# Kernel tuning notes

Hardware: AMD Instinct MI355X
Metric: run time of the kernel (lower is better)

Reference implementation:

```python
import jax, jax.numpy as jnp
import numpy as np

B, T, C, H = 2, 2048, 1024, 16
D = C // H  # head_dim = 64


def setup_inputs() -> dict:
    key = jax.random.key(0)
    k1, k2, k3, k4 = jax.random.split(key, 4)
    x = jax.random.normal(k1, (B, T, C), dtype=jnp.float32)
    # key_padding_mask: True for valid token, False for padding.
    # Use per-example valid lengths so the mask is realistic; every example
    # has length >= 1 so no softmax row is fully masked.
    lengths = jax.random.randint(k2, (B,), T // 2, T + 1)
    key_padding_mask = jnp.arange(T)[None, :] < lengths[:, None]
    Wqkv = jax.random.normal(k3, (3 * C, C), dtype=jnp.float32) * 0.02
    bqkv = jnp.zeros((3 * C,), dtype=jnp.float32)
    Wproj = jax.random.normal(k4, (C, C), dtype=jnp.float32) * 0.02
    bproj = jnp.zeros((C,), dtype=jnp.float32)
    return {"x": x, "key_padding_mask": key_padding_mask,
            "Wqkv": Wqkv, "bqkv": bqkv, "Wproj": Wproj, "bproj": bproj}


def reference(x, key_padding_mask, Wqkv, bqkv, Wproj, bproj):
    # qkv projection (torch Linear: y = x @ W^T + b)
    qkv = jnp.einsum('btc,oc->bto', x, Wqkv) + bqkv          # (B,T,3C)
    q, k, v = jnp.split(qkv, 3, axis=-1)
    q = q.reshape(B, T, H, D)
    k = k.reshape(B, T, H, D)
    v = v.reshape(B, T, H, D)
    scale = 1.0 / np.sqrt(D).astype(np.float32)
    scores = jnp.einsum('bqhd,bkhd->bhqk', q, k) * scale      # (B,H,T,T)
    causal = jnp.tril(jnp.ones((T, T), dtype=bool))           # (T,T)
    mask = causal[None, None, :, :] & key_padding_mask[:, None, None, :]
    scores = jnp.where(mask, scores, -jnp.inf)
    attn = jax.nn.softmax(scores, axis=-1)                    # dropout p=0.0
    out = jnp.einsum('bhqk,bkhd->bqhd', attn, v).reshape(B, T, C)
    out = jnp.einsum('btc,oc->bto', out, Wproj) + bproj
    return out
```

## Files before the change

### kernel.cpp

```cpp
#include <hip/hip_runtime.h>
#include <hip/hip_bf16.h>
#include <stdint.h>

#define B_ 2
#define T_ 2048
#define C_ 1024
#define H_ 16
#define D_ 64

typedef __attribute__((ext_vector_type(8))) short bf16x8;
typedef __attribute__((ext_vector_type(4))) float f32x4;

__device__ __forceinline__ unsigned short f2bf(float f) {
  union { float f; uint32_t u; } c; c.f = f;
  uint32_t r = c.u + 0x7FFFu + ((c.u >> 16) & 1u);
  return (unsigned short)(r >> 16);
}

__device__ __forceinline__ uint32_t pack_bf16x2(float lo, float hi) {
  uint32_t r;
  asm("v_cvt_pk_bf16_f32 %0, %1, %2" : "=v"(r) : "v"(lo), "v"(hi));
  return r;
}

__device__ __forceinline__ void gload_lds16(const unsigned short* g,
                                            unsigned short* l) {
  __builtin_amdgcn_global_load_lds(
      (const __attribute__((address_space(1))) void*)(g),
      (__attribute__((address_space(3))) void*)(l), 16, 0, 0);
}

__global__ void cvt_f32_bf16(const float* __restrict__ s,
                             unsigned short* __restrict__ d, int n4) {
  int i = blockIdx.x * blockDim.x + threadIdx.x;
  if (i >= n4) return;
  float4 v = ((const float4*)s)[i];
  ushort4 o;
  o.x = f2bf(v.x); o.y = f2bf(v.y); o.z = f2bf(v.z); o.w = f2bf(v.w);
  ((ushort4*)d)[i] = o;
}

__global__ void compute_lengths(const unsigned int* __restrict__ mask,
                                int* __restrict__ lens) {
  int lane = threadIdx.x;
  unsigned int w0 = mask[0];
  for (int b = 0; b < B_; ++b) {
    int cnt = 0;
    if (w0 == 1u) {
      for (int t = lane; t < T_; t += 64) cnt += (mask[(size_t)b * T_ + t] != 0u);
    } else if (w0 == 0x3F800000u) {
      const float* mf = (const float*)mask;
      for (int t = lane; t < T_; t += 64) cnt += (mf[(size_t)b * T_ + t] != 0.f);
    } else {
      const unsigned char* mb = (const unsigned char*)mask;
      for (int t = lane; t < T_; t += 64) cnt += (mb[(size_t)b * T_ + t] != 0);
    }
    for (int off = 32; off > 0; off >>= 1) cnt += __shfl_down(cnt, off);
    if (lane == 0) lens[b] = cnt;
  }
}

__global__ __launch_bounds__(256)
void gemm_bt(const unsigned short* __restrict__ A,
             const unsigned short* __restrict__ Bm,
             const float* __restrict__ bias,
             float* __restrict__ outF,
             unsigned short* __restrict__ Qw,
             unsigned short* __restrict__ Kw,
             unsigned short* __restrict__ Vw,
             int N, int K, int mode) {
  __shared__ unsigned short As[128 * 64];
  __shared__ unsigned short Bs[128 * 64];
  const int tid = threadIdx.x;
  const int lane = tid & 63;
  const int w = tid >> 6;
  const int wm = w >> 1, wn = w & 1;
  const int q4 = lane >> 4, l15 = lane & 15;
  const int bm = blockIdx.y * 128;
  const int bn = blockIdx.x * 128;

  f32x4 acc[4][4] = {};

  for (int kt = 0; kt < K; kt += 64) {
#pragma unroll
    for (int i = 0; i < 4; ++i) {
      int r0 = w * 32 + i * 8;
      int row = r0 + (lane >> 3);
      int kc = (lane & 7) ^ (row & 7);
      gload_lds16(A + (size_t)(bm + row) * K + kt + kc * 8, &As[r0 * 64]);
      gload_lds16(Bm + (size_t)(bn + row) * K + kt + kc * 8, &Bs[r0 * 64]);
    }
    __syncthreads();
#pragma unroll
    for (int kk = 0; kk < 2; ++kk) {
      bf16x8 af[4], bfv[4];
#pragma unroll
      for (int mi = 0; mi < 4; ++mi) {
        int row = wm * 64 + mi * 16 + l15;
        int pc = (kk * 4 + q4) ^ (row & 7);
        af[mi] = *(const bf16x8*)(As + (size_t)row * 64 + pc * 8);
      }
#pragma unroll
      for (int ni = 0; ni < 4; ++ni) {
        int row = wn * 64 + ni * 16 + l15;
        int pc = (kk * 4 + q4) ^ (row & 7);
        bfv[ni] = *(const bf16x8*)(Bs + (size_t)row * 64 + pc * 8);
      }
#pragma unroll
      for (int mi = 0; mi < 4; ++mi)
#pragma unroll
        for (int ni = 0; ni < 4; ++ni)
          acc[mi][ni] = __builtin_amdgcn_mfma_f32_16x16x32_bf16(
              af[mi], bfv[ni], acc[mi][ni], 0, 0, 0);
    }
    __syncthreads();
  }

#pragma unroll
  for (int mi = 0; mi < 4; ++mi) {
    const int row0 = bm + wm * 64 + mi * 16 + q4 * 4;
#pragma unroll
    for (int ni = 0; ni < 4; ++ni) {
      const int col = bn + wn * 64 + ni * 16 + l15;
      const float bv = bias[col];
#pragma unroll
      for (int r = 0; r < 4; ++r) {
        const int row = row0 + r;
        float v = acc[mi][ni][r] + bv;
        if (mode == 1) {
          outF[(size_t)row * N + col] = v;
        } else {
          int b = row >> 11, t = row & (T_ - 1);
          int which = col >> 10, c = col & (C_ - 1);
          int h = c >> 6, dd = c & (D_ - 1);
          unsigned short* dst = (which == 0) ? Qw : ((which == 1) ? Kw : Vw);
          if (which == 0) v *= 0.1803368801111243f;
          dst[(((size_t)(b * H_ + h) * T_) + t) * D_ + dd] = f2bf(v);
        }
      }
    }
  }
}

__global__ __launch_bounds__(256)
void transpose_v(const unsigned short* __restrict__ V,
                 unsigned short* __restrict__ Vt) {
  __shared__ unsigned short tile[64][65];
  int bh = blockIdx.y;
  int t0 = blockIdx.x * 64;
  int tid = threadIdx.x;
  int r = tid >> 2, c0 = (tid & 3) * 16;
  const uint4* s4 = (const uint4*)(V + ((size_t)bh * T_ + t0 + r) * D_ + c0);
  union { uint4 v; unsigned short u[8]; } ua, ub;
  ua.v = s4[0]; ub.v = s4[1];
#pragma unroll
  for (int j = 0; j < 8; ++j) {
    tile[r][c0 + j] = ua.u[j];
    tile[r][c0 + 8 + j] = ub.u[j];
  }
  __syncthreads();
  int dd = tid >> 2, tt0 = (tid & 3) * 16;
  union { uint4 v[2]; unsigned short u[16]; } ov;
#pragma unroll
  for (int j = 0; j < 16; ++j) ov.u[j] = tile[tt0 + j][dd];
  uint4* dptr = (uint4*)(Vt + ((size_t)bh * D_ + dd) * T_ + t0 + tt0);
  dptr[0] = ov.v[0];
  dptr[1] = ov.v[1];
}

__global__ __launch_bounds__(512)
void attn_fwd(const unsigned short* __restrict__ Qw,
              const unsigned short* __restrict__ Kw,
              const unsigned short* __restrict__ Vt,
              unsigned short* __restrict__ AO,
              const int* __restrict__ lens) {
  __shared__ unsigned short Ks[2][64 * 64];
  __shared__ unsigned short Vs[2][64 * 64];
  __shared__ unsigned short Pb[8][16 * 64];

  const int bh = blockIdx.y;
  const int b = bh >> 4;
  const int h = bh & 15;
  const int qt = gridDim.x - 1 - blockIdx.x;
  const int q0 = qt * 128;
  const int tid = threadIdx.x;
  const int lane = tid & 63;
  const int w = tid >> 6;
  const int q4 = lane >> 4, l15 = lane & 15;
  const int len = lens[b];

  const unsigned short* Qp = Qw + (size_t)bh * T_ * D_;
  const unsigned short* Kp = Kw + (size_t)bh * T_ * D_;
  const unsigned short* Vp = Vt + (size_t)bh * D_ * T_;
  unsigned short* Pw = &Pb[w][0];

  const int qw0 = q0 + w * 16;
  const int qwmax = qw0 + 15;

  bf16x8 qf[2];
#pragma unroll
  for (int kk = 0; kk < 2; ++kk)
    qf[kk] = *(const bf16x8*)(Qp + (size_t)(qw0 + l15) * D_ + kk * 32 + q4 * 8);

  f32x4 ot[4] = {};
  float m = -INFINITY;
  float lsum = 0.f;

  int kcap = q0 + 127;
  if (kcap > len - 1) kcap = len - 1;
  const int nkt = kcap / 64 + 1;

  const int srow = lane >> 3;
  const int scc = lane & 7;
  const int sr0 = w * 8;
  const int rk = sr0 + srow;
  const int skc = scc ^ (rk & 7);

  gload_lds16(Kp + (size_t)rk * D_ + skc * 8, &Ks[0][sr0 * 64]);
  gload_lds16(Vp + (size_t)rk * T_ + skc * 8, &Vs[0][sr0 * 64]);
  __syncthreads();

  int cur = 0;
  for (int kt = 0; kt < nkt; ++kt) {
    const int kbase = kt * 64;
    if (kt + 1 < nkt) {
      const int kb2 = kbase + 64;
      gload_lds16(Kp + (size_t)(kb2 + rk) * D_ + skc * 8, &Ks[cur ^ 1][sr0 * 64]);
      gload_lds16(Vp + (size_t)rk * T_ + kb2 + skc * 8, &Vs[cur ^ 1][sr0 * 64]);
    }

    if (kbase <= qwmax) {
      f32x4 st[4];
#pragma unroll
      for (int nt = 0; nt < 4; ++nt) {
        bf16x8 kfr0, kfr1;
        {
          int row = nt * 16 + l15;
          int pc0 = q4 ^ (row & 7);
          int pc1 = (4 + q4) ^ (row & 7);
          kfr0 = *(const bf16x8*)(&Ks[cur][row * 64 + pc0 * 8]);
          kfr1 = *(const bf16x8*)(&Ks[cur][row * 64 + pc1 * 8]);
        }
        f32x4 z = {};
        z = __builtin_amdgcn_mfma_f32_16x16x32_bf16(kfr0, qf[0], z, 0, 0, 0);
        z = __builtin_amdgcn_mfma_f32_16x16x32_bf16(kfr1, qf[1], z, 0, 0, 0);
        st[nt] = z;
      }
      const bool interior = (kbase + 63 <= qw0) && (kbase + 63 < len);
      float pmax = -INFINITY;
      if (interior) {
#pragma unroll
        for (int nt = 0; nt < 4; ++nt)
#pragma unroll
          for (int r = 0; r < 4; ++r) pmax = fmaxf(pmax, st[nt][r]);
      } else {
        const int qq = qw0 + l15;
#pragma unroll
        for (int nt = 0; nt < 4; ++nt)
#pragma unroll
          for (int r = 0; r < 4; ++r) {
            int kpos = kbase + nt * 16 + q4 * 4 + r;
            bool ok = (kpos < len) && (kpos <= qq);
            float v = ok ? st[nt][r] : -INFINITY;
            st[nt][r] = v;
            pmax = fmaxf(pmax, v);
          }
      }
      pmax = fmaxf(pmax, __shfl_xor(pmax, 16));
      pmax = fmaxf(pmax, __shfl_xor(pmax, 32));
      if (!__all(pmax <= m + 8.f)) {
        float mn = fmaxf(m, pmax);
        float sc = exp2f(m - mn);
        m = mn;
        lsum *= sc;
#pragma unroll
        for (int dt = 0; dt < 4; ++dt)
#pragma unroll
          for (int r = 0; r < 4; ++r) ot[dt][r] *= sc;
      }
      float psum = 0.f;
#pragma unroll
      for (int nt = 0; nt < 4; ++nt) {
        float p0 = exp2f(st[nt][0] - m);
        float p1 = exp2f(st[nt][1] - m);
        float p2 = exp2f(st[nt][2] - m);
        float p3 = exp2f(st[nt][3] - m);
        psum += (p0 + p1) + (p2 + p3);
        uint32_t w0 = pack_bf16x2(p0, p1);
        uint32_t w1 = pack_bf16x2(p2, p3);
        int c = nt * 4 + q4;
        int phys = c ^ ((l15 & 7) << 1);
        uint2 pr; pr.x = w0; pr.y = w1;
        *(uint2*)(&Pw[l15 * 64 + phys * 4]) = pr;
      }
      psum += __shfl_xor(psum, 16);
      psum += __shfl_xor(psum, 32);
      lsum += psum;
      bf16x8 pt[2];
#pragma unroll
      for (int kk = 0; kk < 2; ++kk) {
        int c0 = kk * 8 + q4 * 2;
        int phys = c0 ^ ((l15 & 7) << 1);
        pt[kk] = *(const bf16x8*)(&Pw[l15 * 64 + phys * 4]);
      }
#pragma unroll
      for (int dt = 0; dt < 4; ++dt) {
        bf16x8 vfr0, vfr1;
        {
          int row = dt * 16 + l15;
          int pc0 = q4 ^ (row & 7);
          int pc1 = (4 + q4) ^ (row & 7);
          vfr0 = *(const bf16x8*)(&Vs[cur][row * 64 + pc0 * 8]);
          vfr1 = *(const bf16x8*)(&Vs[cur][row * 64 + pc1 * 8]);
        }
        ot[dt] = __builtin_amdgcn_mfma_f32_16x16x32_bf16(vfr0, pt[0], ot[dt], 0, 0, 0);
        ot[dt] = __builtin_amdgcn_mfma_f32_16x16x32_bf16(vfr1, pt[1], ot[dt], 0, 0, 0);
      }
    }

    __syncthreads();
    cur ^= 1;
  }

  {
    float inv = 1.f / lsum;
    int qq = qw0 + l15;
#pragma unroll
    for (int dt = 0; dt < 4; ++dt) {
      uint2 pr;
      pr.x = pack_bf16x2(ot[dt][0] * inv, ot[dt][1] * inv);
      pr.y = pack_bf16x2(ot[dt][2] * inv, ot[dt][3] * inv);
      *(uint2*)(&AO[(size_t)(b * T_ + qq) * C_ + h * 64 + dt * 16 + q4 * 4]) = pr;
    }
  }
}

extern "C" void kernel_launch(void* const* d_in, const int* in_sizes, int n_in,
                              void* d_out, int out_size, void* d_ws, size_t ws_size,
                              hipStream_t stream) {
  const float* x = (const float*)d_in[0];
  const unsigned int* mask = (const unsigned int*)d_in[1];
  const float* Wqkv = (const float*)d_in[2];
  const float* bqkv = (const float*)d_in[3];
  const float* Wproj = (const float*)d_in[4];
  const float* bproj = (const float*)d_in[5];
  float* out = (float*)d_out;

  unsigned short* XB = (unsigned short*)d_ws;
  unsigned short* WQ = XB + 4194304;
  unsigned short* WP = WQ + 3145728;
  unsigned short* Qw = WP + 1048576;
  unsigned short* Kw = Qw + 4194304;
  unsigned short* Vw = Kw + 4194304;
  unsigned short* Vt = Vw + 4194304;
  unsigned short* AO = Vt + 4194304;
  int* lens = (int*)(AO + 4194304);

  cvt_f32_bf16<<<4096, 256, 0, stream>>>(x, XB, 1048576);
  cvt_f32_bf16<<<3072, 256, 0, stream>>>(Wqkv, WQ, 786432);
  cvt_f32_bf16<<<1024, 256, 0, stream>>>(Wproj, WP, 262144);
  compute_lengths<<<1, 64, 0, stream>>>(mask, lens);

  gemm_bt<<<dim3(3072 / 128, 4096 / 128), 256, 0, stream>>>(
      XB, WQ, bqkv, nullptr, Qw, Kw, Vw, 3072, 1024, 0);

  transpose_v<<<dim3(T_ / 64, B_ * H_), 256, 0, stream>>>(Vw, Vt);

  attn_fwd<<<dim3(T_ / 128, B_ * H_), 512, 0, stream>>>(Qw, Kw, Vt, AO, lens);

  gemm_bt<<<dim3(1024 / 128, 4096 / 128), 256, 0, stream>>>(
      AO, WP, bproj, out, nullptr, nullptr, nullptr, 1024, 1024, 1);
}
```

Before: 232.3 us.

## Shrink attention query tile to 64 rows and merge bf16 conversion kernels

The attention kernel now uses 64-query blocks with 4 warps instead of 128-query blocks with 8 warps, doubling the grid. Each warp loads two 8-row slices of K/V per tile to keep the 64-row tile load cooperative. This is meant to improve load balance under the causal mask and raise occupancy, at the cost of reloading K/V tiles twice as often across blocks. The three fp32-to-bf16 conversion launches are also merged into one kernel to save launch overhead.

```diff
diff --git a/kernel.cpp b/kernel.cpp
--- a/kernel.cpp
+++ b/kernel.cpp
@@ -30,14 +30,24 @@
       (__attribute__((address_space(3))) void*)(l), 16, 0, 0);
 }
 
-__global__ void cvt_f32_bf16(const float* __restrict__ s,
-                             unsigned short* __restrict__ d, int n4) {
-  int i = blockIdx.x * blockDim.x + threadIdx.x;
-  if (i >= n4) return;
-  float4 v = ((const float4*)s)[i];
+#define N4_X 1048576
+#define N4_WQ 786432
+#define N4_WP 262144
+__global__ void cvt_all(const float* __restrict__ x,
+                        const float* __restrict__ wqkv,
+                        const float* __restrict__ wproj,
+                        unsigned short* __restrict__ xb,
+                        unsigned short* __restrict__ wq,
+                        unsigned short* __restrict__ wp) {
+  int i = blockIdx.x * 256 + threadIdx.x;
+  const float* s; unsigned short* d; int j;
+  if (i < N4_X) { s = x; d = xb; j = i; }
+  else if (i < N4_X + N4_WQ) { s = wqkv; d = wq; j = i - N4_X; }
+  else { s = wproj; d = wp; j = i - (N4_X + N4_WQ); }
+  float4 v = ((const float4*)s)[j];
   ushort4 o;
   o.x = f2bf(v.x); o.y = f2bf(v.y); o.z = f2bf(v.z); o.w = f2bf(v.w);
-  ((ushort4*)d)[i] = o;
+  ((ushort4*)d)[j] = o;
 }
 
 __global__ void compute_lengths(const unsigned int* __restrict__ mask,
@@ -168,7 +178,7 @@
   dptr[1] = ov.v[1];
 }
 
-__global__ __launch_bounds__(512)
+__global__ __launch_bounds__(256)
 void attn_fwd(const unsigned short* __restrict__ Qw,
               const unsigned short* __restrict__ Kw,
               const unsigned short* __restrict__ Vt,
@@ -176,13 +186,13 @@
               const int* __restrict__ lens) {
   __shared__ unsigned short Ks[2][64 * 64];
   __shared__ unsigned short Vs[2][64 * 64];
-  __shared__ unsigned short Pb[8][16 * 64];
+  __shared__ unsigned short Pb[4][16 * 64];
 
   const int bh = blockIdx.y;
   const int b = bh >> 4;
   const int h = bh & 15;
-  const int qt = gridDim.x - 1 - blockIdx.x;
-  const int q0 = qt * 128;
+  const int qs = 31 - blockIdx.x;
+  const int q0 = qs * 64;
   const int tid = threadIdx.x;
   const int lane = tid & 63;
   const int w = tid >> 6;
@@ -206,18 +216,21 @@
   float m = -INFINITY;
   float lsum = 0.f;
 
-  int kcap = q0 + 127;
+  int kcap = q0 + 63;
   if (kcap > len - 1) kcap = len - 1;
   const int nkt = kcap / 64 + 1;
 
   const int srow = lane >> 3;
   const int scc = lane & 7;
-  const int sr0 = w * 8;
-  const int rk = sr0 + srow;
-  const int skc = scc ^ (rk & 7);
-
-  gload_lds16(Kp + (size_t)rk * D_ + skc * 8, &Ks[0][sr0 * 64]);
-  gload_lds16(Vp + (size_t)rk * T_ + skc * 8, &Vs[0][sr0 * 64]);
+
+#pragma unroll
+  for (int i = 0; i < 2; ++i) {
+    int r0 = w * 16 + i * 8;
+    int rk = r0 + srow;
+    int kc = scc ^ (rk & 7);
+    gload_lds16(Kp + (size_t)rk * D_ + kc * 8, &Ks[0][r0 * 64]);
+    gload_lds16(Vp + (size_t)rk * T_ + kc * 8, &Vs[0][r0 * 64]);
+  }
   __syncthreads();
 
   int cur = 0;
@@ -225,8 +238,14 @@
     const int kbase = kt * 64;
     if (kt + 1 < nkt) {
       const int kb2 = kbase + 64;
-      gload_lds16(Kp + (size_t)(kb2 + rk) * D_ + skc * 8, &Ks[cur ^ 1][sr0 * 64]);
-      gload_lds16(Vp + (size_t)rk * T_ + kb2 + skc * 8, &Vs[cur ^ 1][sr0 * 64]);
+#pragma unroll
+      for (int i = 0; i < 2; ++i) {
+        int r0 = w * 16 + i * 8;
+        int rk = r0 + srow;
+        int kc = scc ^ (rk & 7);
+        gload_lds16(Kp + (size_t)(kb2 + rk) * D_ + kc * 8, &Ks[cur ^ 1][r0 * 64]);
+        gload_lds16(Vp + (size_t)rk * T_ + kb2 + kc * 8, &Vs[cur ^ 1][r0 * 64]);
+      }
     }
 
     if (kbase <= qwmax) {
@@ -356,9 +375,7 @@
   unsigned short* AO = Vt + 4194304;
   int* lens = (int*)(AO + 4194304);
 
-  cvt_f32_bf16<<<4096, 256, 0, stream>>>(x, XB, 1048576);
-  cvt_f32_bf16<<<3072, 256, 0, stream>>>(Wqkv, WQ, 786432);
-  cvt_f32_bf16<<<1024, 256, 0, stream>>>(Wproj, WP, 262144);
+  cvt_all<<<8192, 256, 0, stream>>>(x, Wqkv, Wproj, XB, WQ, WP);
   compute_lengths<<<1, 64, 0, stream>>>(mask, lens);
 
   gemm_bt<<<dim3(3072 / 128, 4096 / 128), 256, 0, stream>>>(
@@ -366,7 +383,7 @@
 
   transpose_v<<<dim3(T_ / 64, B_ * H_), 256, 0, stream>>>(Vw, Vt);
 
-  attn_fwd<<<dim3(T_ / 128, B_ * H_), 512, 0, stream>>>(Qw, Kw, Vt, AO, lens);
+  attn_fwd<<<dim3(32, B_ * H_), 256, 0, stream>>>(Qw, Kw, Vt, AO, lens);
 
   gemm_bt<<<dim3(1024 / 128, 4096 / 128), 256, 0, stream>>>(
       AO, WP, bproj, out, nullptr, nullptr, nullptr, 1024, 1024, 1);
```

Result: no change. 235.8 us (+1.5%).
